# Kernel tuning notes

Hardware: AMD Instinct MI355X
Metric: run time of the kernel (lower is better)

Reference implementation:

```python
import jax, jax.numpy as jnp
import numpy as np

SCALE = 10.0
TEMP = 0.5
SIM_TH = 0.7
EPOCH = 1
KL_WEIGHT = max(0.5 * (1 - EPOCH / 60), 0.1)
NEG_INF = -1e30


def _normalize(x, eps=1e-12):
    n = jnp.linalg.norm(x, axis=-1, keepdims=True)
    return x / jnp.maximum(n, eps)


def setup_inputs() -> dict:
    key = jax.random.key(0)
    ks = jax.random.split(key, 6)
    P, B, D, N, K = 4, 128, 512, 32768, 10
    # 0.02 scale keeps pairwise distances O(1) so exp(-SCALE*dist) does not underflow
    feature = jax.random.normal(ks[0], (P, B, D), jnp.float32) * 0.02
    text_feature = jax.random.normal(ks[1], (B, P, D), jnp.float32) * 0.02
    centers = jax.random.normal(ks[2], (P, N, D), jnp.float32) * 0.02
    position = jax.random.randint(ks[3], (B,), 0, N)
    cross_indices = jax.random.randint(ks[4], (B, K), 0, N)
    vid = jax.random.randint(ks[5], (N,), 0, 751)
    return {"feature": feature, "text_feature": text_feature, "centers": centers,
            "position": position, "cross_indices": cross_indices, "vid": vid}


def _align_loss(feature, text_feature):
    # feature: [P,B,D]; text_feature: [B,P,D] (detached in original)
    img = _normalize(feature)
    txt = _normalize(jax.lax.stop_gradient(jnp.transpose(text_feature, (1, 0, 2))))
    img_sim = jnp.einsum('pbd,pcd->pbc', img, img) / TEMP   # [P,B,B]
    txt_sim = jnp.einsum('pbd,pcd->pbc', txt, txt) / TEMP
    mask = (img_sim > SIM_TH) & (txt_sim > SIM_TH)
    valid = mask.any(-1)                                   # [P,B] row/col validity
    colm = valid[:, None, :]                               # mask over columns
    il = jnp.where(colm, img_sim, NEG_INF)
    tl = jnp.where(colm, txt_sim, NEG_INF)
    img_logp = jax.nn.log_softmax(il, -1)
    txt_logp = jax.nn.log_softmax(tl, -1)                  # fully detached (txt detached)
    txt_prob = jnp.exp(txt_logp)
    img_logp_sg = jax.lax.stop_gradient(img_logp)
    img_prob = jnp.exp(img_logp_sg)
    # F.kl_div(input=log q, target=p) = sum p*(log p - log q), batchmean over valid rows
    kl1 = jnp.sum(jnp.where(colm, txt_prob * (txt_logp - img_logp), 0.0), -1)      # [P,B]
    kl2 = jnp.sum(jnp.where(colm, img_prob * (img_logp_sg - txt_logp), 0.0), -1)
    nvalid = valid.sum(-1)                                 # [P]
    r1 = jnp.sum(jnp.where(valid, kl1, 0.0), -1)
    r2 = jnp.sum(jnp.where(valid, kl2, 0.0), -1)
    per_part = 0.5 * (r1 + r2) / jnp.maximum(nvalid, 1)
    return jnp.sum(jnp.where(nvalid > 0, per_part, 0.0))


def _contrastive_loss(feature, centers, position, cross_indices):
    P, B, D = feature.shape
    N = centers.shape[1]
    pos_feats = jnp.take(centers, cross_indices, axis=1)   # [P,B,K,D]
    fn2 = jnp.sum(feature * feature, -1)                   # [P,B]
    pn2 = jnp.sum(pos_feats * pos_feats, -1)               # [P,B,K]
    pd2 = fn2[..., None] + pn2 - 2.0 * jnp.einsum('pbd,pbkd->pbk', feature, pos_feats)
    pos_dist = jnp.sqrt(jnp.maximum(pd2, 1e-12))           # [P,B,K]
    cn2 = jnp.sum(centers * centers, -1)                   # [P,N]
    nd2 = fn2[..., None] + cn2[:, None, :] - 2.0 * jnp.einsum('pbd,pnd->pbn', feature, centers)
    neg_dist = jnp.sqrt(jnp.maximum(nd2, 1e-12))           # [P,B,N]
    neg_mask = (jnp.ones((N,), bool)
                .at[cross_indices.reshape(-1)].set(False)
                .at[position].set(False))
    x = jnp.log(jnp.sum(jnp.exp(-SCALE * pos_dist), -1))   # [P,B]
    ey = jnp.exp(-SCALE * neg_dist) * neg_mask[None, None, :].astype(neg_dist.dtype)
    y = jnp.log(jnp.sum(ey, -1))                           # [P,B]
    l = jnp.sum(y - x, -1) / B                             # per-part, div by feature.size(1)
    l = jnp.where(jnp.isnan(l), 0.0, l)
    return jnp.sum(l) / P


def reference(feature, text_feature, centers, position, cross_indices, vid):
    align_loss = _align_loss(feature, text_feature)
    contrastive_loss = _contrastive_loss(feature, centers, position, cross_indices)
    total_loss = contrastive_loss + KL_WEIGHT * align_loss
    pos_vid = jnp.take(vid, cross_indices, axis=0)         # [B,K]
    return total_loss, contrastive_loss, align_loss, pos_vid
```

## Files before the change

kernel.cpp:

```cpp
#include <hip/hip_runtime.h>
#include <hip/hip_bf16.h>
#include <math.h>

#define P_ 4
#define B_ 128
#define D_ 512
#define N_ 32768
#define K_ 10
#define TNB 128
#define NT2 (N_ / TNB)
#define BK2 32
#define NCH (D_ / BK2)

typedef __attribute__((ext_vector_type(8))) short bf16x8;
typedef __attribute__((ext_vector_type(4))) float f32x4;

static __device__ __forceinline__ float block_sum_128(float v, float* sh) {
    const int t = threadIdx.x;
    sh[t] = v; __syncthreads();
    #pragma unroll
    for (int s = 64; s > 0; s >>= 1) { if (t < s) sh[t] += sh[t + s]; __syncthreads(); }
    float r = sh[0]; __syncthreads();
    return r;
}

static __device__ __forceinline__ uint2 pack_bf16x4(float4 v) {
    union { __hip_bfloat162 h; unsigned u; } lo, hi;
    lo.h = __float22bfloat162_rn(make_float2(v.x, v.y));
    hi.h = __float22bfloat162_rn(make_float2(v.z, v.w));
    uint2 r; r.x = lo.u; r.y = hi.u;
    return r;
}

__global__ __launch_bounds__(256) void prep_kernel(const float* __restrict__ feature,
                                                   unsigned short* __restrict__ Abf,
                                                   float* __restrict__ fn2) {
    const int pb = blockIdx.x;
    const int t = threadIdx.x;
    const float2 v = *(const float2*)(feature + (size_t)pb * D_ + 2 * t);
    union { __hip_bfloat162 h; unsigned u; } pk;
    pk.h = __float22bfloat162_rn(make_float2(v.x, v.y));
    ((unsigned*)Abf)[(size_t)pb * (D_ / 2) + t] = pk.u;
    __shared__ float sred[256];
    sred[t] = v.x * v.x + v.y * v.y;
    __syncthreads();
    #pragma unroll
    for (int s = 128; s > 0; s >>= 1) { if (t < s) sred[t] += sred[t + s]; __syncthreads(); }
    if (t == 0) fn2[pb] = sred[0];
}

__global__ __launch_bounds__(128) void sim_kernel(
    const float* __restrict__ feature,
    const float* __restrict__ text_feature,
    float* __restrict__ img_sim,
    float* __restrict__ txt_sim,
    float* __restrict__ validf,
    float* __restrict__ Ssum) {
    const int p = blockIdx.x;
    const int b0 = blockIdx.y * 2;
    const int c = threadIdx.x;
    if (blockIdx.y == 0) Ssum[p * B_ + c] = 0.0f;
    __shared__ float ai[2][D_];
    __shared__ float at[2][D_];
    __shared__ float cinv_i[128];
    __shared__ float cinv_t[128];
    __shared__ int flags[2];
    #pragma unroll
    for (int i = 0; i < 8; ++i) {
        int idx = c + i * 128;
        int row = idx >> 9, d = idx & 511;
        ai[row][d] = feature[(size_t)(p * B_ + b0 + row) * D_ + d];
        at[row][d] = text_feature[((size_t)(b0 + row) * P_ + p) * D_ + d];
    }
    if (c < 2) flags[c] = 0;
    __syncthreads();
    float di[2] = {0, 0};
    float dt[2] = {0, 0};
    float ssi = 0.0f, sst = 0.0f;
    const float* fc = feature + (size_t)(p * B_ + c) * D_;
    const float* tc = text_feature + ((size_t)c * P_ + p) * D_;
    for (int d = 0; d < D_; d += 4) {
        float4 vi = *(const float4*)(fc + d);
        float4 vt = *(const float4*)(tc + d);
        ssi += vi.x * vi.x + vi.y * vi.y + vi.z * vi.z + vi.w * vi.w;
        sst += vt.x * vt.x + vt.y * vt.y + vt.z * vt.z + vt.w * vt.w;
        #pragma unroll
        for (int i = 0; i < 2; ++i) {
            float4 a4 = *(const float4*)&ai[i][d];
            float4 t4 = *(const float4*)&at[i][d];
            di[i] += a4.x * vi.x + a4.y * vi.y + a4.z * vi.z + a4.w * vi.w;
            dt[i] += t4.x * vt.x + t4.y * vt.y + t4.z * vt.z + t4.w * vt.w;
        }
    }
    cinv_i[c] = 1.0f / fmaxf(sqrtf(ssi), 1e-12f);
    cinv_t[c] = 1.0f / fmaxf(sqrtf(sst), 1e-12f);
    __syncthreads();
    #pragma unroll
    for (int i = 0; i < 2; ++i) {
        float is = 2.0f * di[i] * cinv_i[b0 + i] * cinv_i[c];
        float ts = 2.0f * dt[i] * cinv_t[b0 + i] * cinv_t[c];
        img_sim[(size_t)(p * B_ + b0 + i) * B_ + c] = is;
        txt_sim[(size_t)(p * B_ + b0 + i) * B_ + c] = ts;
        if (is > 0.7f && ts > 0.7f) flags[i] = 1;
    }
    __syncthreads();
    if (c < 2) validf[p * B_ + b0 + c] = (float)flags[c];
}

__global__ __launch_bounds__(256) void kl_kernel(
    const float* __restrict__ img_sim,
    const float* __restrict__ txt_sim,
    const float* __restrict__ validf,
    float* __restrict__ klrow) {
    const int l = threadIdx.x & 63;
    const int wv = threadIdx.x >> 6;
    const int p = blockIdx.x;
    const int r = blockIdx.y * 4 + wv;
    const size_t base = (size_t)(p * B_ + r) * B_;
    const bool v0 = validf[p * B_ + l] > 0.5f;
    const bool v1 = validf[p * B_ + 64 + l] > 0.5f;
    const float il0 = v0 ? img_sim[base + l] : -1e30f;
    const float il1 = v1 ? img_sim[base + 64 + l] : -1e30f;
    const float tl0 = v0 ? txt_sim[base + l] : -1e30f;
    const float tl1 = v1 ? txt_sim[base + 64 + l] : -1e30f;
    float mi = fmaxf(il0, il1), mt = fmaxf(tl0, tl1);
    #pragma unroll
    for (int off = 32; off > 0; off >>= 1) {
        mi = fmaxf(mi, __shfl_xor(mi, off));
        mt = fmaxf(mt, __shfl_xor(mt, off));
    }
    float si = expf(il0 - mi) + expf(il1 - mi);
    float st = expf(tl0 - mt) + expf(tl1 - mt);
    #pragma unroll
    for (int off = 32; off > 0; off >>= 1) {
        si += __shfl_xor(si, off);
        st += __shfl_xor(st, off);
    }
    const float lsei = mi + logf(si);
    const float lset = mt + logf(st);
    float term = 0.0f;
    if (v0) {
        float lpi = il0 - lsei, lpt = tl0 - lset;
        term += expf(lpt) * (lpt - lpi) + expf(lpi) * (lpi - lpt);
    }
    if (v1) {
        float lpi = il1 - lsei, lpt = tl1 - lset;
        term += expf(lpt) * (lpt - lpi) + expf(lpi) * (lpi - lpt);
    }
    #pragma unroll
    for (int off = 32; off > 0; off >>= 1) term += __shfl_xor(term, off);
    if (l == 0) klrow[p * B_ + r] = (validf[p * B_ + r] > 0.5f) ? term : 0.0f;
}

__global__ void posx_kernel(const float* __restrict__ feature,
                            const float* __restrict__ centers,
                            const int* __restrict__ cross,
                            float* __restrict__ xarr) {
    const int pb = blockIdx.x;
    const int p = pb >> 7, b = pb & 127;
    const int l = threadIdx.x;
    const float* f = feature + (size_t)pb * D_;
    float4 f0 = *(const float4*)(f + l * 4);
    float4 f1 = *(const float4*)(f + 256 + l * 4);
    float fs = f0.x * f0.x + f0.y * f0.y + f0.z * f0.z + f0.w * f0.w
             + f1.x * f1.x + f1.y * f1.y + f1.z * f1.z + f1.w * f1.w;
    #pragma unroll
    for (int off = 32; off > 0; off >>= 1) fs += __shfl_down(fs, off);
    float ex = 0.0f;
    #pragma unroll
    for (int k = 0; k < K_; ++k) {
        int idx = cross[b * K_ + k];
        const float* cp = centers + ((size_t)p * N_ + idx) * D_;
        float4 c0 = *(const float4*)(cp + l * 4);
        float4 c1 = *(const float4*)(cp + 256 + l * 4);
        float dot = f0.x * c0.x + f0.y * c0.y + f0.z * c0.z + f0.w * c0.w
                  + f1.x * c1.x + f1.y * c1.y + f1.z * c1.z + f1.w * c1.w;
        float pn2 = c0.x * c0.x + c0.y * c0.y + c0.z * c0.z + c0.w * c0.w
                  + c1.x * c1.x + c1.y * c1.y + c1.z * c1.z + c1.w * c1.w;
        #pragma unroll
        for (int off = 32; off > 0; off >>= 1) {
            dot += __shfl_down(dot, off);
            pn2 += __shfl_down(pn2, off);
        }
        if (l == 0) {
            float d2 = fs + pn2 - 2.0f * dot;
            ex += expf(-10.0f * sqrtf(fmaxf(d2, 1e-12f)));
        }
    }
    if (l == 0) xarr[pb] = logf(ex);
}

static __device__ __forceinline__ void load_set(
    const unsigned short* Ap, const float* Bp, int kk,
    bf16x8 (&aX)[4], float4 (&b0X)[4], float4 (&b1X)[4]) {
    #pragma unroll
    for (int i = 0; i < 4; ++i)
        aX[i] = *(const bf16x8*)(Ap + (size_t)(i * 16) * D_ + kk);
    #pragma unroll
    for (int j = 0; j < 4; ++j) {
        const float* r = Bp + (size_t)(j * 16) * D_ + kk;
        b0X[j] = *(const float4*)(r);
        b1X[j] = *(const float4*)(r + 4);
    }
}

static __device__ __forceinline__ void compute_set(
    const bf16x8 (&aX)[4], const float4 (&b0X)[4], const float4 (&b1X)[4],
    f32x4 (&acc)[4][4], float (&cn2p)[4]) {
    bf16x8 bfr[4];
    #pragma unroll
    for (int j = 0; j < 4; ++j) {
        cn2p[j] += b0X[j].x * b0X[j].x + b0X[j].y * b0X[j].y
                 + b0X[j].z * b0X[j].z + b0X[j].w * b0X[j].w
                 + b1X[j].x * b1X[j].x + b1X[j].y * b1X[j].y
                 + b1X[j].z * b1X[j].z + b1X[j].w * b1X[j].w;
        uint2 lo = pack_bf16x4(b0X[j]);
        uint2 hi = pack_bf16x4(b1X[j]);
        union { unsigned u[4]; bf16x8 v; } m;
        m.u[0] = lo.x; m.u[1] = lo.y; m.u[2] = hi.x; m.u[3] = hi.y;
        bfr[j] = m.v;
    }
    #pragma unroll
    for (int i = 0; i < 4; ++i)
        #pragma unroll
        for (int j = 0; j < 4; ++j)
            acc[i][j] = __builtin_amdgcn_mfma_f32_16x16x32_bf16(
                aX[i], bfr[j], acc[i][j], 0, 0, 0);
}

__global__ __launch_bounds__(256) void neg_mfma_kernel(
    const unsigned short* __restrict__ Abf,
    const float* __restrict__ centers,
    const float* __restrict__ fn2,
    const int* __restrict__ cross,
    const int* __restrict__ position,
    float* __restrict__ Ssum) {
    const int tile = blockIdx.x;
    const int p = blockIdx.y;
    const int n0g = tile * TNB;
    const int t = threadIdx.x;
    const int l = t & 63;
    const int w = t >> 6;
    const int m0w = (w & 1) * 64;
    const int n0w = (w >> 1) * 64;

    __shared__ float red[128];
    __shared__ float msk[128];
    __shared__ float fn2s[128];

    if (t < 128) { red[t] = 0.0f; msk[t] = 1.0f; fn2s[t] = fn2[p * B_ + t]; }
    __syncthreads();
    for (int i = t; i < B_ * K_ + B_; i += 256) {
        const int v = (i < B_ * K_) ? cross[i] : position[i - B_ * K_];
        const unsigned rr = (unsigned)(v - n0g);
        if (rr < (unsigned)TNB) msk[rr] = 0.0f;
    }
    __syncthreads();

    const int fr = l & 15;
    const int kg = l >> 4;
    const unsigned short* Ap = Abf + ((size_t)p * B_ + m0w + fr) * D_ + kg * 8;
    const float* Bp = centers + ((size_t)p * N_ + n0g + n0w + fr) * D_ + kg * 8;

    f32x4 acc[4][4];
    #pragma unroll
    for (int i = 0; i < 4; ++i)
        #pragma unroll
        for (int j = 0; j < 4; ++j) acc[i][j] = (f32x4)0.0f;
    float cn2p[4] = {0.0f, 0.0f, 0.0f, 0.0f};

    bf16x8 aA[4], aB[4];
    float4 b0A[4], b1A[4], b0B[4], b1B[4];

    load_set(Ap, Bp, 0, aA, b0A, b1A);
    #pragma unroll 1
    for (int c = 0; c < NCH; c += 2) {
        load_set(Ap, Bp, (c + 1) * BK2, aB, b0B, b1B);
        compute_set(aA, b0A, b1A, acc, cn2p);
        if (c + 2 < NCH) load_set(Ap, Bp, (c + 2) * BK2, aA, b0A, b1A);
        compute_set(aB, b0B, b1B, acc, cn2p);
    }

    float c2l[4], mkl[4];
    #pragma unroll
    for (int j = 0; j < 4; ++j) {
        float s = cn2p[j];
        s += __shfl_xor(s, 16);
        s += __shfl_xor(s, 32);
        c2l[j] = s;
        mkl[j] = msk[n0w + j * 16 + fr];
    }

    #pragma unroll
    for (int i = 0; i < 4; ++i) {
        #pragma unroll
        for (int r = 0; r < 4; ++r) {
            const int row = m0w + i * 16 + kg * 4 + r;
            const float fv = fn2s[row];
            float s = 0.0f;
            #pragma unroll
            for (int j = 0; j < 4; ++j) {
                const float nd2 = fv + c2l[j] - 2.0f * acc[i][j][r];
                s += mkl[j] * __expf(-10.0f * sqrtf(fmaxf(nd2, 1e-12f)));
            }
            s += __shfl_xor(s, 1); s += __shfl_xor(s, 2);
            s += __shfl_xor(s, 4); s += __shfl_xor(s, 8);
            if (fr == 0) atomicAdd(&red[row], s);
        }
    }
    __syncthreads();
    if (t < 128) atomicAdd(&Ssum[p * B_ + t], red[t]);
}

__global__ void final_kernel(const float* __restrict__ validf,
                             const float* __restrict__ klrow,
                             const float* __restrict__ xarr,
                             const float* __restrict__ Ssum,
                             const int* __restrict__ cross,
                             const int* __restrict__ vid,
                             float* __restrict__ out) {
    const int t = threadIdx.x;
    __shared__ float sh[128];
    __shared__ float accum[2];
    if (t == 0) { accum[0] = 0.0f; accum[1] = 0.0f; }
    __syncthreads();
    for (int p = 0; p < P_; ++p) {
        float nv = block_sum_128(validf[p * B_ + t], sh);
        float ks = block_sum_128(klrow[p * B_ + t], sh);
        float dv = logf(Ssum[p * B_ + t]) - xarr[p * B_ + t];
        float ds = block_sum_128(dv, sh);
        if (t == 0) {
            float lp = ds / (float)B_;
            if (!(lp != lp)) accum[0] += lp;
            if (nv > 0.5f) accum[1] += 0.5f * ks / fmaxf(nv, 1.0f);
        }
        __syncthreads();
    }
    if (t == 0) {
        float contrastive = accum[0] / (float)P_;
        float align = accum[1];
        out[1] = contrastive;
        out[2] = align;
        out[0] = contrastive + 0.49166666666666664f * align;
    }
    #pragma unroll
    for (int k = 0; k < K_; ++k) {
        const int i = k * 128 + t;
        out[3 + i] = (float)vid[cross[i]];
    }
}

extern "C" void kernel_launch(void* const* d_in, const int* in_sizes, int n_in,
                              void* d_out, int out_size, void* d_ws, size_t ws_size,
                              hipStream_t stream) {
    const float* feature      = (const float*)d_in[0];
    const float* text_feature = (const float*)d_in[1];
    const float* centers      = (const float*)d_in[2];
    const int*   position     = (const int*)d_in[3];
    const int*   cross        = (const int*)d_in[4];
    const int*   vid          = (const int*)d_in[5];
    float* out = (float*)d_out;

    float* ws      = (float*)d_ws;
    float* img_sim = ws;
    float* txt_sim = img_sim + (size_t)P_ * B_ * B_;
    float* validf  = txt_sim + (size_t)P_ * B_ * B_;
    float* klrow   = validf + P_ * B_;
    float* xarr    = klrow + P_ * B_;
    float* Ssum    = xarr + P_ * B_;
    float* fn2     = Ssum + P_ * B_;
    unsigned short* Abf = (unsigned short*)(fn2 + P_ * B_);

    prep_kernel<<<P_ * B_, 256, 0, stream>>>(feature, Abf, fn2);
    sim_kernel<<<dim3(P_, B_ / 2), 128, 0, stream>>>(feature, text_feature,
                                                     img_sim, txt_sim, validf, Ssum);
    kl_kernel<<<dim3(P_, B_ / 4), 256, 0, stream>>>(img_sim, txt_sim, validf, klrow);
    posx_kernel<<<P_ * B_, 64, 0, stream>>>(feature, centers, cross, xarr);
    neg_mfma_kernel<<<dim3(NT2, P_), 256, 0, stream>>>(Abf, centers, fn2, cross,
                                                       position, Ssum);
    final_kernel<<<1, 128, 0, stream>>>(validf, klrow, xarr, Ssum, cross, vid, out);
}
```

Baseline: 457.3 us.

## Stage centers tile in LDS as bf16 and split work by rows across waves

The negative-distance MFMA kernel now stages each 32-column group of centers into double-buffered shared memory as bf16, with the squared norms precomputed during staging. Each wave then owns 32 feature rows and reads B fragments from LDS, overlapping global loads for the next group with MFMA on the current one. Before, each wave loaded its own 64-column slice of centers directly from global memory and converted it in registers, so every column was fetched and converted by two waves. The new scheme removes that duplicated global traffic and conversion, at the cost of extra LDS writes and barriers and reading A fragments from global memory on each group.

Result: slower. 550.0 us (+20.3%).

```diff
diff --git a/kernel.cpp b/kernel.cpp
--- a/kernel.cpp
+++ b/kernel.cpp
@@ -9,8 +9,9 @@
 #define K_ 10
 #define TNB 128
 #define NT2 (N_ / TNB)
-#define BK2 32
-#define NCH (D_ / BK2)
+#define NG 32
+#define NGR (TNB / NG)
+#define BSTR 520
 
 typedef __attribute__((ext_vector_type(8))) short bf16x8;
 typedef __attribute__((ext_vector_type(4))) float f32x4;
@@ -190,44 +191,6 @@
     if (l == 0) xarr[pb] = logf(ex);
 }
 
-static __device__ __forceinline__ void load_set(
-    const unsigned short* Ap, const float* Bp, int kk,
-    bf16x8 (&aX)[4], float4 (&b0X)[4], float4 (&b1X)[4]) {
-    #pragma unroll
-    for (int i = 0; i < 4; ++i)
-        aX[i] = *(const bf16x8*)(Ap + (size_t)(i * 16) * D_ + kk);
-    #pragma unroll
-    for (int j = 0; j < 4; ++j) {
-        const float* r = Bp + (size_t)(j * 16) * D_ + kk;
-        b0X[j] = *(const float4*)(r);
-        b1X[j] = *(const float4*)(r + 4);
-    }
-}
-
-static __device__ __forceinline__ void compute_set(
-    const bf16x8 (&aX)[4], const float4 (&b0X)[4], const float4 (&b1X)[4],
-    f32x4 (&acc)[4][4], float (&cn2p)[4]) {
-    bf16x8 bfr[4];
-    #pragma unroll
-    for (int j = 0; j < 4; ++j) {
-        cn2p[j] += b0X[j].x * b0X[j].x + b0X[j].y * b0X[j].y
-                 + b0X[j].z * b0X[j].z + b0X[j].w * b0X[j].w
-                 + b1X[j].x * b1X[j].x + b1X[j].y * b1X[j].y
-                 + b1X[j].z * b1X[j].z + b1X[j].w * b1X[j].w;
-        uint2 lo = pack_bf16x4(b0X[j]);
-        uint2 hi = pack_bf16x4(b1X[j]);
-        union { unsigned u[4]; bf16x8 v; } m;
-        m.u[0] = lo.x; m.u[1] = lo.y; m.u[2] = hi.x; m.u[3] = hi.y;
-        bfr[j] = m.v;
-    }
-    #pragma unroll
-    for (int i = 0; i < 4; ++i)
-        #pragma unroll
-        for (int j = 0; j < 4; ++j)
-            acc[i][j] = __builtin_amdgcn_mfma_f32_16x16x32_bf16(
-                aX[i], bfr[j], acc[i][j], 0, 0, 0);
-}
-
 __global__ __launch_bounds__(256) void neg_mfma_kernel(
     const unsigned short* __restrict__ Abf,
     const float* __restrict__ centers,
@@ -241,75 +204,135 @@
     const int t = threadIdx.x;
     const int l = t & 63;
     const int w = t >> 6;
-    const int m0w = (w & 1) * 64;
-    const int n0w = (w >> 1) * 64;
-
-    __shared__ float red[128];
+    const int fr = l & 15;
+    const int kg = l >> 4;
+    const int il = l & 7;
+    const int rw = l >> 3;
+
+    __shared__ unsigned short Bs[2][NG * BSTR];
+    __shared__ float cn2g[2][NG];
     __shared__ float msk[128];
-    __shared__ float fn2s[128];
-
-    if (t < 128) { red[t] = 0.0f; msk[t] = 1.0f; fn2s[t] = fn2[p * B_ + t]; }
+
+    if (t < 128) msk[t] = 1.0f;
     __syncthreads();
     for (int i = t; i < B_ * K_ + B_; i += 256) {
         const int v = (i < B_ * K_) ? cross[i] : position[i - B_ * K_];
         const unsigned rr = (unsigned)(v - n0g);
         if (rr < (unsigned)TNB) msk[rr] = 0.0f;
     }
-    __syncthreads();
-
-    const int fr = l & 15;
-    const int kg = l >> 4;
-    const unsigned short* Ap = Abf + ((size_t)p * B_ + m0w + fr) * D_ + kg * 8;
-    const float* Bp = centers + ((size_t)p * N_ + n0g + n0w + fr) * D_ + kg * 8;
-
-    f32x4 acc[4][4];
-    #pragma unroll
-    for (int i = 0; i < 4; ++i)
-        #pragma unroll
-        for (int j = 0; j < 4; ++j) acc[i][j] = (f32x4)0.0f;
-    float cn2p[4] = {0.0f, 0.0f, 0.0f, 0.0f};
-
-    bf16x8 aA[4], aB[4];
-    float4 b0A[4], b1A[4], b0B[4], b1B[4];
-
-    load_set(Ap, Bp, 0, aA, b0A, b1A);
-    #pragma unroll 1
-    for (int c = 0; c < NCH; c += 2) {
-        load_set(Ap, Bp, (c + 1) * BK2, aB, b0B, b1B);
-        compute_set(aA, b0A, b1A, acc, cn2p);
-        if (c + 2 < NCH) load_set(Ap, Bp, (c + 2) * BK2, aA, b0A, b1A);
-        compute_set(aB, b0B, b1B, acc, cn2p);
-    }
-
-    float c2l[4], mkl[4];
-    #pragma unroll
-    for (int j = 0; j < 4; ++j) {
-        float s = cn2p[j];
-        s += __shfl_xor(s, 16);
-        s += __shfl_xor(s, 32);
-        c2l[j] = s;
-        mkl[j] = msk[n0w + j * 16 + fr];
-    }
-
-    #pragma unroll
-    for (int i = 0; i < 4; ++i) {
-        #pragma unroll
-        for (int r = 0; r < 4; ++r) {
-            const int row = m0w + i * 16 + kg * 4 + r;
-            const float fv = fn2s[row];
-            float s = 0.0f;
+
+    const int srow = w * 8 + rw;
+
+#define STAGE_LOAD(g, h, vv) \
+    { const float* rp = centers + ((size_t)p * N_ + n0g + (g) * NG + srow) * D_; \
+      _Pragma("unroll") \
+      for (int q = 0; q < 8; ++q) \
+        vv[q] = *(const float4*)(rp + ((h) * 64 + q * 8 + il) * 4); }
+
+#define STAGE_WRITE(h, vv, buf, s2) \
+    { _Pragma("unroll") \
+      for (int q = 0; q < 8; ++q) { \
+        s2 += vv[q].x * vv[q].x + vv[q].y * vv[q].y \
+            + vv[q].z * vv[q].z + vv[q].w * vv[q].w; \
+        *(uint2*)&Bs[buf][srow * BSTR + ((h) * 64 + q * 8 + il) * 4] = pack_bf16x4(vv[q]); \
+      } }
+
+#define STAGE_FIN(buf, s2) \
+    { float s = s2; \
+      s += __shfl_xor(s, 1); s += __shfl_xor(s, 2); s += __shfl_xor(s, 4); \
+      if (il == 0) cn2g[buf][srow] = s; }
+
+    const unsigned short* Ap0 = Abf + ((size_t)p * B_ + w * 32 + fr) * D_ + kg * 8;
+    const unsigned short* Ap1 = Ap0 + (size_t)16 * D_;
+
+    float fvv0[4], fvv1[4];
+    #pragma unroll
+    for (int r = 0; r < 4; ++r) {
+        fvv0[r] = fn2[p * B_ + w * 32 + kg * 4 + r];
+        fvv1[r] = fn2[p * B_ + w * 32 + 16 + kg * 4 + r];
+    }
+
+    f32x4 acc00, acc01, acc10, acc11;
+    float ssum0[4] = {0, 0, 0, 0};
+    float ssum1[4] = {0, 0, 0, 0};
+
+    float4 vst[8];
+    float s2a;
+
+    s2a = 0.0f;
+    STAGE_LOAD(0, 0, vst)
+    STAGE_WRITE(0, vst, 0, s2a)
+    STAGE_LOAD(0, 1, vst)
+    STAGE_WRITE(1, vst, 0, s2a)
+    STAGE_FIN(0, s2a)
+    __syncthreads();
+
+#define COMPUTE_CHUNKS(buf, c0, c1) \
+    _Pragma("unroll") \
+    for (int c = (c0); c < (c1); ++c) { \
+        bf16x8 a0 = *(const bf16x8*)(Ap0 + c * 32); \
+        bf16x8 a1 = *(const bf16x8*)(Ap1 + c * 32); \
+        bf16x8 b0 = *(const bf16x8*)&Bs[buf][fr * BSTR + kg * 8 + c * 32]; \
+        bf16x8 b1 = *(const bf16x8*)&Bs[buf][(fr + 16) * BSTR + kg * 8 + c * 32]; \
+        acc00 = __builtin_amdgcn_mfma_f32_16x16x32_bf16(a0, b0, acc00, 0, 0, 0); \
+        acc01 = __builtin_amdgcn_mfma_f32_16x16x32_bf16(a0, b1, acc01, 0, 0, 0); \
+        acc10 = __builtin_amdgcn_mfma_f32_16x16x32_bf16(a1, b0, acc10, 0, 0, 0); \
+        acc11 = __builtin_amdgcn_mfma_f32_16x16x32_bf16(a1, b1, acc11, 0, 0, 0); \
+    }
+
+    for (int g = 0; g < NGR; ++g) {
+        const int cur = g & 1, nxt = cur ^ 1;
+        acc00 = (f32x4)0.0f; acc01 = (f32x4)0.0f;
+        acc10 = (f32x4)0.0f; acc11 = (f32x4)0.0f;
+        s2a = 0.0f;
+        if (g + 1 < NGR) STAGE_LOAD(g + 1, 0, vst)
+        COMPUTE_CHUNKS(cur, 0, 8)
+        if (g + 1 < NGR) {
+            STAGE_WRITE(0, vst, nxt, s2a)
+            STAGE_LOAD(g + 1, 1, vst)
+        }
+        COMPUTE_CHUNKS(cur, 8, 16)
+        if (g + 1 < NGR) {
+            STAGE_WRITE(1, vst, nxt, s2a)
+            STAGE_FIN(nxt, s2a)
+        }
+        {
+            const float c20 = cn2g[cur][fr];
+            const float c21 = cn2g[cur][fr + 16];
+            const float mk0 = msk[g * NG + fr];
+            const float mk1 = msk[g * NG + 16 + fr];
             #pragma unroll
-            for (int j = 0; j < 4; ++j) {
-                const float nd2 = fv + c2l[j] - 2.0f * acc[i][j][r];
-                s += mkl[j] * __expf(-10.0f * sqrtf(fmaxf(nd2, 1e-12f)));
+            for (int r = 0; r < 4; ++r) {
+                float nd;
+                nd = fvv0[r] + c20 - 2.0f * acc00[r];
+                ssum0[r] += mk0 * __expf(-10.0f * sqrtf(fmaxf(nd, 1e-12f)));
+                nd = fvv0[r] + c21 - 2.0f * acc01[r];
+                ssum0[r] += mk1 * __expf(-10.0f * sqrtf(fmaxf(nd, 1e-12f)));
+                nd = fvv1[r] + c20 - 2.0f * acc10[r];
+                ssum1[r] += mk0 * __expf(-10.0f * sqrtf(fmaxf(nd, 1e-12f)));
+                nd = fvv1[r] + c21 - 2.0f * acc11[r];
+                ssum1[r] += mk1 * __expf(-10.0f * sqrtf(fmaxf(nd, 1e-12f)));
             }
-            s += __shfl_xor(s, 1); s += __shfl_xor(s, 2);
-            s += __shfl_xor(s, 4); s += __shfl_xor(s, 8);
-            if (fr == 0) atomicAdd(&red[row], s);
-        }
-    }
-    __syncthreads();
-    if (t < 128) atomicAdd(&Ssum[p * B_ + t], red[t]);
+        }
+        asm volatile("s_waitcnt lgkmcnt(0)\n\ts_barrier" ::: "memory");
+    }
+
+#undef STAGE_LOAD
+#undef STAGE_WRITE
+#undef STAGE_FIN
+#undef COMPUTE_CHUNKS
+
+    #pragma unroll
+    for (int r = 0; r < 4; ++r) {
+        float v0 = ssum0[r];
+        v0 += __shfl_xor(v0, 1); v0 += __shfl_xor(v0, 2);
+        v0 += __shfl_xor(v0, 4); v0 += __shfl_xor(v0, 8);
+        if (fr == 0) atomicAdd(&Ssum[p * B_ + w * 32 + kg * 4 + r], v0);
+        float v1 = ssum1[r];
+        v1 += __shfl_xor(v1, 1); v1 += __shfl_xor(v1, 2);
+        v1 += __shfl_xor(v1, 4); v1 += __shfl_xor(v1, 8);
+        if (fr == 0) atomicAdd(&Ssum[p * B_ + w * 32 + 16 + kg * 4 + r], v1);
+    }
 }
 
 __global__ void final_kernel(const float* __restrict__ validf,
```

## Stage GEMM tiles through LDS via async global_load_lds with swizzled layout

Applied to the files above, without the earlier changes.

The negative-distance MFMA kernel used to load A (bf16 features) and B (fp32 centers) fragments straight from global memory into registers, so waves sharing a tile loaded duplicate data. Each tile chunk is now copied into double-buffered shared memory with direct global-to-LDS loads under an XOR swizzle, and the MFMA fragments are read back from LDS. This removes redundant global traffic and register pressure from register-level prefetching. In exchange it adds a block-wide barrier per K chunk and about 48KB of LDS, which may lower occupancy.

Measured after the change: 445.2 us. 1.03x faster.

```diff
diff --git a/kernel.cpp b/kernel.cpp
--- a/kernel.cpp
+++ b/kernel.cpp
@@ -15,6 +15,10 @@
 typedef __attribute__((ext_vector_type(8))) short bf16x8;
 typedef __attribute__((ext_vector_type(4))) float f32x4;
 
+#define GLD(g, l) __builtin_amdgcn_global_load_lds( \
+    (const __attribute__((address_space(1))) void*)(g), \
+    (__attribute__((address_space(3))) void*)(l), 16, 0, 0)
+
 static __device__ __forceinline__ float block_sum_128(float v, float* sh) {
     const int t = threadIdx.x;
     sh[t] = v; __syncthreads();
@@ -24,12 +28,10 @@
     return r;
 }
 
-static __device__ __forceinline__ uint2 pack_bf16x4(float4 v) {
-    union { __hip_bfloat162 h; unsigned u; } lo, hi;
-    lo.h = __float22bfloat162_rn(make_float2(v.x, v.y));
-    hi.h = __float22bfloat162_rn(make_float2(v.z, v.w));
-    uint2 r; r.x = lo.u; r.y = hi.u;
-    return r;
+static __device__ __forceinline__ unsigned cvt2bf(float a, float b) {
+    union { __hip_bfloat162 h; unsigned u; } p;
+    p.h = __float22bfloat162_rn(make_float2(a, b));
+    return p.u;
 }
 
 __global__ __launch_bounds__(256) void prep_kernel(const float* __restrict__ feature,
@@ -38,9 +40,7 @@
     const int pb = blockIdx.x;
     const int t = threadIdx.x;
     const float2 v = *(const float2*)(feature + (size_t)pb * D_ + 2 * t);
-    union { __hip_bfloat162 h; unsigned u; } pk;
-    pk.h = __float22bfloat162_rn(make_float2(v.x, v.y));
-    ((unsigned*)Abf)[(size_t)pb * (D_ / 2) + t] = pk.u;
+    ((unsigned*)Abf)[(size_t)pb * (D_ / 2) + t] = cvt2bf(v.x, v.y);
     __shared__ float sred[256];
     sred[t] = v.x * v.x + v.y * v.y;
     __syncthreads();
@@ -190,44 +190,6 @@
     if (l == 0) xarr[pb] = logf(ex);
 }
 
-static __device__ __forceinline__ void load_set(
-    const unsigned short* Ap, const float* Bp, int kk,
-    bf16x8 (&aX)[4], float4 (&b0X)[4], float4 (&b1X)[4]) {
-    #pragma unroll
-    for (int i = 0; i < 4; ++i)
-        aX[i] = *(const bf16x8*)(Ap + (size_t)(i * 16) * D_ + kk);
-    #pragma unroll
-    for (int j = 0; j < 4; ++j) {
-        const float* r = Bp + (size_t)(j * 16) * D_ + kk;
-        b0X[j] = *(const float4*)(r);
-        b1X[j] = *(const float4*)(r + 4);
-    }
-}
-
-static __device__ __forceinline__ void compute_set(
-    const bf16x8 (&aX)[4], const float4 (&b0X)[4], const float4 (&b1X)[4],
-    f32x4 (&acc)[4][4], float (&cn2p)[4]) {
-    bf16x8 bfr[4];
-    #pragma unroll
-    for (int j = 0; j < 4; ++j) {
-        cn2p[j] += b0X[j].x * b0X[j].x + b0X[j].y * b0X[j].y
-                 + b0X[j].z * b0X[j].z + b0X[j].w * b0X[j].w
-                 + b1X[j].x * b1X[j].x + b1X[j].y * b1X[j].y
-                 + b1X[j].z * b1X[j].z + b1X[j].w * b1X[j].w;
-        uint2 lo = pack_bf16x4(b0X[j]);
-        uint2 hi = pack_bf16x4(b1X[j]);
-        union { unsigned u[4]; bf16x8 v; } m;
-        m.u[0] = lo.x; m.u[1] = lo.y; m.u[2] = hi.x; m.u[3] = hi.y;
-        bfr[j] = m.v;
-    }
-    #pragma unroll
-    for (int i = 0; i < 4; ++i)
-        #pragma unroll
-        for (int j = 0; j < 4; ++j)
-            acc[i][j] = __builtin_amdgcn_mfma_f32_16x16x32_bf16(
-                aX[i], bfr[j], acc[i][j], 0, 0, 0);
-}
-
 __global__ __launch_bounds__(256) void neg_mfma_kernel(
     const unsigned short* __restrict__ Abf,
     const float* __restrict__ centers,
@@ -243,7 +205,11 @@
     const int w = t >> 6;
     const int m0w = (w & 1) * 64;
     const int n0w = (w >> 1) * 64;
-
+    const int fr = l & 15;
+    const int kg = l >> 4;
+
+    __shared__ float Bsf[2][128 * 32];
+    __shared__ unsigned short Ash[2][128 * 32];
     __shared__ float red[128];
     __shared__ float msk[128];
     __shared__ float fn2s[128];
@@ -255,12 +221,20 @@
         const unsigned rr = (unsigned)(v - n0g);
         if (rr < (unsigned)TNB) msk[rr] = 0.0f;
     }
-    __syncthreads();
-
-    const int fr = l & 15;
-    const int kg = l >> 4;
-    const unsigned short* Ap = Abf + ((size_t)p * B_ + m0w + fr) * D_ + kg * 8;
-    const float* Bp = centers + ((size_t)p * N_ + n0g + n0w + fr) * D_ + kg * 8;
+
+    const float* gB = centers + ((size_t)p * N_ + n0g + w * 32 + (l >> 3)) * D_
+                    + ((l & 7) ^ (l >> 3)) * 4;
+    const unsigned short* gA = Abf + ((size_t)p * B_ + w * 32 + (l >> 2)) * D_
+                             + ((l & 3) ^ ((l >> 2) & 3)) * 8;
+
+#define STAGE(cc, buf) { \
+    _Pragma("unroll") \
+    for (int q = 0; q < 4; ++q) \
+        GLD(gB + (size_t)q * 8 * D_ + (cc) * 32, &Bsf[buf][(w * 4 + q) * 256]); \
+    _Pragma("unroll") \
+    for (int q = 0; q < 2; ++q) \
+        GLD(gA + (size_t)q * 16 * D_ + (cc) * 32, &Ash[buf][(w * 2 + q) * 512]); \
+  }
 
     f32x4 acc[4][4];
     #pragma unroll
@@ -269,17 +243,45 @@
         for (int j = 0; j < 4; ++j) acc[i][j] = (f32x4)0.0f;
     float cn2p[4] = {0.0f, 0.0f, 0.0f, 0.0f};
 
-    bf16x8 aA[4], aB[4];
-    float4 b0A[4], b1A[4], b0B[4], b1B[4];
-
-    load_set(Ap, Bp, 0, aA, b0A, b1A);
+    const int akslot = kg ^ (fr & 3);
+    const int bslot0 = (2 * kg) ^ (fr & 7);
+    const int bslot1 = bslot0 ^ 1;
+
+    STAGE(0, 0)
+    __syncthreads();
+
     #pragma unroll 1
-    for (int c = 0; c < NCH; c += 2) {
-        load_set(Ap, Bp, (c + 1) * BK2, aB, b0B, b1B);
-        compute_set(aA, b0A, b1A, acc, cn2p);
-        if (c + 2 < NCH) load_set(Ap, Bp, (c + 2) * BK2, aA, b0A, b1A);
-        compute_set(aB, b0B, b1B, acc, cn2p);
-    }
+    for (int c = 0; c < NCH; ++c) {
+        const int cur = c & 1;
+        if (c + 1 < NCH) STAGE(c + 1, cur ^ 1)
+        bf16x8 af[4];
+        #pragma unroll
+        for (int i = 0; i < 4; ++i)
+            af[i] = *(const bf16x8*)&Ash[cur][(m0w + i * 16 + fr) * 32 + akslot * 8];
+        bf16x8 bfr[4];
+        #pragma unroll
+        for (int j = 0; j < 4; ++j) {
+            const int row = n0w + j * 16 + fr;
+            f32x4 lo = *(const f32x4*)&Bsf[cur][row * 32 + bslot0 * 4];
+            f32x4 hi = *(const f32x4*)&Bsf[cur][row * 32 + bslot1 * 4];
+            cn2p[j] += lo[0] * lo[0] + lo[1] * lo[1] + lo[2] * lo[2] + lo[3] * lo[3]
+                     + hi[0] * hi[0] + hi[1] * hi[1] + hi[2] * hi[2] + hi[3] * hi[3];
+            union { unsigned u[4]; bf16x8 v; } m;
+            m.u[0] = cvt2bf(lo[0], lo[1]);
+            m.u[1] = cvt2bf(lo[2], lo[3]);
+            m.u[2] = cvt2bf(hi[0], hi[1]);
+            m.u[3] = cvt2bf(hi[2], hi[3]);
+            bfr[j] = m.v;
+        }
+        #pragma unroll
+        for (int i = 0; i < 4; ++i)
+            #pragma unroll
+            for (int j = 0; j < 4; ++j)
+                acc[i][j] = __builtin_amdgcn_mfma_f32_16x16x32_bf16(
+                    af[i], bfr[j], acc[i][j], 0, 0, 0);
+        __syncthreads();
+    }
+#undef STAGE
 
     float c2l[4], mkl[4];
     #pragma unroll
```
